# Performance work log

Hardware: AMD Instinct MI355X
Metric: run time of the kernel (lower is better)

Reference implementation:

```python
import jax, jax.numpy as jnp
import numpy as np

N_NODES = 50000
D = 128
L = 3  # layers
R = 4  # relations
E = 200000  # edges per relation
LN_EPS = 1e-5
NEG_SLOPE = 0.2


def setup_inputs() -> dict:
    key = jax.random.key(0)
    ks = jax.random.split(key, 12)
    s = 1.0 / np.sqrt(D)  # xavier-ish scale
    return {
        "h": jax.random.normal(ks[0], (N_NODES, D), jnp.float32),
        "edge_src": jax.random.randint(ks[1], (R, E), 0, N_NODES, jnp.int32),
        "edge_dst": jax.random.randint(ks[2], (R, E), 0, N_NODES, jnp.int32),
        "W_src": jax.random.normal(ks[3], (L, R, D, D), jnp.float32) * s,
        "W_dst": jax.random.normal(ks[4], (L, R, D, D), jnp.float32) * s,
        "attn_l": jax.random.normal(ks[5], (L, R, D), jnp.float32) * s,
        "attn_r": jax.random.normal(ks[6], (L, R, D), jnp.float32) * s,
        "gat_bias": jax.random.normal(ks[7], (L, R, D), jnp.float32) * 0.02,
        "ntype_bias": jax.random.normal(ks[8], (L, D), jnp.float32) * 0.02,
        "ln_gamma": jnp.ones((L, D), jnp.float32),
        "ln_beta": jnp.zeros((L, D), jnp.float32),
    }


def _gat_rel(x, Wsrc, Wdst, al, ar, b, src, dst):
    # single-head DGL GATConv with bipartite (src, dst) feats (same node set here)
    n = x.shape[0]
    hs = x @ Wsrc  # [N, D] projected source feats
    hd = x @ Wdst  # [N, D] projected dest feats
    el = (hs * al).sum(-1)  # [N]
    er = (hd * ar).sum(-1)  # [N]
    e = jax.nn.leaky_relu(el[src] + er[dst], NEG_SLOPE)  # [E]
    # edge softmax over incoming edges of each dst node
    m = jax.lax.stop_gradient(jax.ops.segment_max(e, dst, num_segments=n))
    a = jnp.exp(e - m[dst])
    denom = jax.ops.segment_sum(a, dst, num_segments=n)
    w = a / denom[dst]  # [E] attention weights
    out = jax.ops.segment_sum(hs[src] * w[:, None], dst, num_segments=n)  # [N, D]
    return out + b


def _layer_norm(x, g, b):
    mu = x.mean(-1, keepdims=True)
    var = ((x - mu) ** 2).mean(-1, keepdims=True)
    return (x - mu) * jax.lax.rsqrt(var + LN_EPS) * g + b


def reference(h, edge_src, edge_dst, W_src, W_dst, attn_l, attn_r,
              gat_bias, ntype_bias, ln_gamma, ln_beta):
    x = h
    n_layers = W_src.shape[0]
    gat_vmapped = jax.vmap(_gat_rel, in_axes=(None, 0, 0, 0, 0, 0, 0, 0))
    for l in range(n_layers):
        rel_out = gat_vmapped(x, W_src[l], W_dst[l], attn_l[l], attn_r[l],
                              gat_bias[l], edge_src, edge_dst)  # [R, N, D]
        hsum = rel_out.sum(0) + ntype_bias[l]  # HeteroGraphConv 'sum' + ntype bias
        if l < n_layers - 1:
            hsum = jax.nn.relu(hsum)  # activation on all but final layer
        # mean over heads (num_heads=1) is identity; then per-layer LayerNorm
        x = _layer_norm(hsum, ln_gamma[l], ln_beta[l])
    return x
```

## Files before the change

### kernel.cpp

```cpp
#include <hip/hip_runtime.h>

#define NN 50000
#define DIM 128
#define NREL 4
#define NEDGE 200000
#define NLAYER 3
#define SNB 196
#define NODES_PER_BLK 32

typedef short s16x8 __attribute__((ext_vector_type(8)));
typedef float f32x4 __attribute__((ext_vector_type(4)));

__device__ __forceinline__ unsigned short f2bf(float f) {
    union { float f; unsigned u; } c; c.f = f;
    unsigned u = c.u + 0x7fffu + ((c.u >> 16) & 1u);
    return (unsigned short)(u >> 16);
}
__device__ __forceinline__ float lo_bf(unsigned u) {
    union { float f; unsigned u; } c; c.u = u << 16; return c.f;
}
__device__ __forceinline__ float hi_bf(unsigned u) {
    union { float f; unsigned u; } c; c.u = u & 0xffff0000u; return c.f;
}

__global__ __launch_bounds__(256) void k_constf(float* __restrict__ out, int n, float v) {
    int i = blockIdx.x * 256 + threadIdx.x;
    if (i < n) out[i] = v;
}

__global__ __launch_bounds__(256) void k_count(const int* __restrict__ dst, int* __restrict__ counts) {
    int r = blockIdx.y;
    int i = blockIdx.x * 256 + threadIdx.x;
    if (i < NEDGE) {
        int d = dst[r * NEDGE + i];
        if ((unsigned)d < NN) atomicAdd(&counts[r * NN + d], 1);
    }
}

__global__ __launch_bounds__(256) void k_s1(const int* __restrict__ counts, int* __restrict__ bsum) {
    int r = blockIdx.y, b = blockIdx.x;
    int i = b * 256 + threadIdx.x;
    int v = (i < NN) ? counts[r * NN + i] : 0;
    #pragma unroll
    for (int m = 1; m < 64; m <<= 1) v += __shfl_xor(v, m);
    __shared__ int ws[4];
    int wid = threadIdx.x >> 6, lane = threadIdx.x & 63;
    if (lane == 0) ws[wid] = v;
    __syncthreads();
    if (threadIdx.x == 0) bsum[r * SNB + b] = ws[0] + ws[1] + ws[2] + ws[3];
}

__global__ __launch_bounds__(256) void k_s2(const int* __restrict__ bsum, int* __restrict__ boff) {
    int r = threadIdx.x >> 6;
    int lane = threadIdx.x & 63;
    int carry = 0;
    for (int c0 = 0; c0 < SNB; c0 += 64) {
        int b = c0 + lane;
        int v = (b < SNB) ? bsum[r * SNB + b] : 0;
        int inc = v;
        #pragma unroll
        for (int d = 1; d < 64; d <<= 1) {
            int t = __shfl_up(inc, d);
            if (lane >= d) inc += t;
        }
        if (b < SNB) boff[r * SNB + b] = carry + inc - v;
        carry += __shfl(inc, 63);
    }
}

__global__ __launch_bounds__(256) void k_s3(const int* __restrict__ counts, const int* __restrict__ boff,
                                            int* __restrict__ row_ptr, int* __restrict__ nxt) {
    int r = blockIdx.y, b = blockIdx.x;
    int i = b * 256 + threadIdx.x;
    int v = (i < NN) ? counts[r * NN + i] : 0;
    int lane = threadIdx.x & 63, wid = threadIdx.x >> 6;
    int inc = v;
    #pragma unroll
    for (int d = 1; d < 64; d <<= 1) {
        int t = __shfl_up(inc, d);
        if (lane >= d) inc += t;
    }
    __shared__ int ws[4];
    if (lane == 63) ws[wid] = inc;
    __syncthreads();
    int woff = 0;
    #pragma unroll
    for (int w = 0; w < 4; ++w) woff += (w < wid) ? ws[w] : 0;
    if (i < NN) {
        int ex = boff[r * SNB + b] + woff + inc - v;
        row_ptr[r * (NN + 1) + i] = ex;
        nxt[r * NN + i] = ex;
    }
    if (b == 0 && threadIdx.x == 0) row_ptr[r * (NN + 1) + NN] = NEDGE;
}

__global__ __launch_bounds__(256) void k_fill(const int* __restrict__ src, const int* __restrict__ dst,
                                              int* __restrict__ nxt, int* __restrict__ csr) {
    int r = blockIdx.y;
    int i = blockIdx.x * 256 + threadIdx.x;
    if (i < NEDGE) {
        int d = dst[r * NEDGE + i];
        if ((unsigned)d >= NN) return;
        int pos = atomicAdd(&nxt[r * NN + d], 1);
        if ((unsigned)pos < NEDGE) csr[r * NEDGE + pos] = src[r * NEDGE + i];
    }
}

__global__ __launch_bounds__(256) void k_prep(const float* __restrict__ Wsrc,
                                              const float* __restrict__ Wdst,
                                              const float* __restrict__ al,
                                              const float* __restrict__ ar,
                                              const float* __restrict__ ntb,
                                              const float* __restrict__ gb,
                                              const float* __restrict__ x,
                                              unsigned short* __restrict__ wf,
                                              float* __restrict__ wl,
                                              float* __restrict__ wr,
                                              float* __restrict__ biasc,
                                              unsigned short* __restrict__ xb) {
    int b = blockIdx.x;
    const int PL = NLAYER * 512;
    if (b < PL) {
        int l = b / 512;
        int t = b % 512;
        if (t < 256) {
            int idx = t * 256 + threadIdx.x;
            int jj = idx & 7, lane = (idx >> 3) & 63, s = (idx >> 9) & 3, tt = (idx >> 11) & 7, r = idx >> 14;
            int k = s * 32 + ((lane >> 4) << 3) + jj;
            int n = tt * 16 + (lane & 15);
            wf[l * 65536 + idx] = f2bf(Wsrc[((size_t)(l * NREL + r) * DIM + k) * DIM + n]);
        } else if (t < 384) {
            int gw = (t - 256) * 4 + (threadIdx.x >> 6);
            int lane = threadIdx.x & 63;
            int r = gw >> 7, k = gw & 127;
            const float* wrow = Wsrc + (((size_t)(l * NREL + r) * DIM + k) * DIM);
            const float* arow = al + (l * NREL + r) * DIM;
            float s = wrow[lane * 2] * arow[lane * 2] + wrow[lane * 2 + 1] * arow[lane * 2 + 1];
            #pragma unroll
            for (int m = 1; m < 64; m <<= 1) s += __shfl_xor(s, m);
            if (lane == 0) wl[l * 512 + gw] = s;
        } else {
            int gw = (t - 384) * 4 + (threadIdx.x >> 6);
            int lane = threadIdx.x & 63;
            int r = gw >> 7, k = gw & 127;
            const float* wrow = Wdst + (((size_t)(l * NREL + r) * DIM + k) * DIM);
            const float* arow = ar + (l * NREL + r) * DIM;
            float s = wrow[lane * 2] * arow[lane * 2] + wrow[lane * 2 + 1] * arow[lane * 2 + 1];
            #pragma unroll
            for (int m = 1; m < 64; m <<= 1) s += __shfl_xor(s, m);
            if (lane == 0) wr[l * 512 + gw] = s;
        }
    } else if (b < PL + 2) {
        int t = (b - PL) * 256 + threadIdx.x;
        if (t < NLAYER * DIM) {
            int l = t >> 7, k = t & 127;
            float s = ntb[t];
            #pragma unroll
            for (int r = 0; r < NREL; ++r) s += gb[(l * NREL + r) * DIM + k];
            biasc[t] = s;
        }
    } else {
        int i = ((b - PL - 2) * 256 + threadIdx.x) * 4;
        f32x4 v = *(const f32x4*)(x + i);
        unsigned short o[4];
        #pragma unroll
        for (int j = 0; j < 4; ++j) o[j] = f2bf(v[j]);
        *(ushort2*)(xb + i) = make_ushort2(o[0], o[1]);
        *(ushort2*)(xb + i + 2) = make_ushort2(o[2], o[3]);
    }
}

__global__ __launch_bounds__(256) void k_er0(const float* __restrict__ x,
                                             const float* __restrict__ wl,
                                             const float* __restrict__ wr,
                                             float* __restrict__ el,
                                             float* __restrict__ er) {
    int oct = threadIdx.x >> 3, ol = threadIdx.x & 7;
    int n = blockIdx.x * 32 + oct;
    if (n >= NN) return;
    int f0 = ol * 16;
    const float* xp = x + (size_t)n * DIM + f0;
    f32x4 xv[4];
    #pragma unroll
    for (int k = 0; k < 4; ++k) xv[k] = *(const f32x4*)(xp + 4 * k);
    #pragma unroll
    for (int r = 0; r < NREL; ++r) {
        float sl = 0.f, sr = 0.f;
        #pragma unroll
        for (int k = 0; k < 4; ++k) {
            f32x4 lv = *(const f32x4*)(wl + r * DIM + f0 + 4 * k);
            f32x4 rv = *(const f32x4*)(wr + r * DIM + f0 + 4 * k);
            sl += xv[k][0] * lv[0] + xv[k][1] * lv[1] + xv[k][2] * lv[2] + xv[k][3] * lv[3];
            sr += xv[k][0] * rv[0] + xv[k][1] * rv[1] + xv[k][2] * rv[2] + xv[k][3] * rv[3];
        }
        sl += __shfl_xor(sl, 1); sl += __shfl_xor(sl, 2); sl += __shfl_xor(sl, 4);
        sr += __shfl_xor(sr, 1); sr += __shfl_xor(sr, 2); sr += __shfl_xor(sr, 4);
        if (ol == 0) { el[r * NN + n] = sl; er[r * NN + n] = sr; }
    }
}

__global__ __launch_bounds__(256) void k_fused(const unsigned short* __restrict__ xb,
                                               const float* __restrict__ el,
                                               const float* __restrict__ er,
                                               const int* __restrict__ row_ptr,
                                               const int* __restrict__ csr,
                                               const unsigned short* __restrict__ wf,
                                               const float* __restrict__ biasc,
                                               const float* __restrict__ lng,
                                               const float* __restrict__ lnb,
                                               const float* __restrict__ wl,
                                               const float* __restrict__ wr,
                                               float* __restrict__ dout,
                                               unsigned short* __restrict__ xb2,
                                               float* __restrict__ el2,
                                               float* __restrict__ er2,
                                               int l, int last) {
    __shared__ s16x8 lds_a[2 * 16 * 64];
    int tid = threadIdx.x;

    for (int p = 0; p < 2; ++p) {
        int pair = tid >> 2;
        int ol   = tid & 3;
        int nd   = pair >> 2;
        int r    = pair & 3;
        int n    = blockIdx.x * NODES_PER_BLK + p * 16 + nd;
        int f0   = ol * 32;

        int valid = (n < NN);
        int nc = valid ? n : 0;
        int start = row_ptr[r * (NN + 1) + nc];
        int end   = valid ? row_ptr[r * (NN + 1) + nc + 1] : start;
        if (start < 0) start = 0;
        if (end > NEDGE) end = NEDGE;
        int deg = end - start;

        float ern = er[r * NN + nc];
        const int* cp = csr + r * NEDGE;
        const float* elp = el + r * NN;

        f32x4 av[8] = {{0,0,0,0},{0,0,0,0},{0,0,0,0},{0,0,0,0},
                       {0,0,0,0},{0,0,0,0},{0,0,0,0},{0,0,0,0}};
        float denom = 0.f;
        if (deg > 0) {
            int s0 = cp[start]; if ((unsigned)s0 >= NN) s0 = 0;
            float e0 = elp[s0];
            const uint4* hp = (const uint4*)(xb + (size_t)s0 * DIM + f0);
            uint4 xa = hp[0], xbv = hp[1], xc = hp[2], xd = hp[3];
            for (int e = 0; e < deg; ++e) {
                int i1 = start + e + 1; i1 = (i1 < end) ? i1 : start;
                int s1 = cp[i1]; if ((unsigned)s1 >= NN) s1 = 0;
                float e1 = elp[s1];
                const uint4* hp1 = (const uint4*)(xb + (size_t)s1 * DIM + f0);
                uint4 ya = hp1[0], yb = hp1[1], yc = hp1[2], yd = hp1[3];

                float ev = e0 + ern;
                ev = ev >= 0.f ? ev : 0.2f * ev;
                ev = fminf(fmaxf(ev, -60.f), 60.f);
                float pw = __expf(ev);
                denom += pw;
                av[0][0] += pw * lo_bf(xa.x); av[0][1] += pw * hi_bf(xa.x);
                av[0][2] += pw * lo_bf(xa.y); av[0][3] += pw * hi_bf(xa.y);
                av[1][0] += pw * lo_bf(xa.z); av[1][1] += pw * hi_bf(xa.z);
                av[1][2] += pw * lo_bf(xa.w); av[1][3] += pw * hi_bf(xa.w);
                av[2][0] += pw * lo_bf(xbv.x); av[2][1] += pw * hi_bf(xbv.x);
                av[2][2] += pw * lo_bf(xbv.y); av[2][3] += pw * hi_bf(xbv.y);
                av[3][0] += pw * lo_bf(xbv.z); av[3][1] += pw * hi_bf(xbv.z);
                av[3][2] += pw * lo_bf(xbv.w); av[3][3] += pw * hi_bf(xbv.w);
                av[4][0] += pw * lo_bf(xc.x); av[4][1] += pw * hi_bf(xc.x);
                av[4][2] += pw * lo_bf(xc.y); av[4][3] += pw * hi_bf(xc.y);
                av[5][0] += pw * lo_bf(xc.z); av[5][1] += pw * hi_bf(xc.z);
                av[5][2] += pw * lo_bf(xc.w); av[5][3] += pw * hi_bf(xc.w);
                av[6][0] += pw * lo_bf(xd.x); av[6][1] += pw * hi_bf(xd.x);
                av[6][2] += pw * lo_bf(xd.y); av[6][3] += pw * hi_bf(xd.y);
                av[7][0] += pw * lo_bf(xd.z); av[7][1] += pw * hi_bf(xd.z);
                av[7][2] += pw * lo_bf(xd.w); av[7][3] += pw * hi_bf(xd.w);
                e0 = e1; xa = ya; xbv = yb; xc = yc; xd = yd;
            }
        }
        float inv = (deg > 0) ? (1.0f / denom) : 0.f;
        #pragma unroll
        for (int q = 0; q < 4; ++q) {
            s16x8 o;
            #pragma unroll
            for (int j = 0; j < 4; ++j) {
                o[j]     = (short)f2bf(av[2 * q][j] * inv);
                o[j + 4] = (short)f2bf(av[2 * q + 1][j] * inv);
            }
            lds_a[p * 1024 + (r * 4 + ol) * 64 + q * 16 + nd] = o;
        }
    }
    __syncthreads();

    int wv = tid >> 6, lane = tid & 63;
    int quad = lane >> 4, n16 = lane & 15;
    f32x4 acc00 = {0.f, 0.f, 0.f, 0.f}, acc01 = {0.f, 0.f, 0.f, 0.f};
    f32x4 acc10 = {0.f, 0.f, 0.f, 0.f}, acc11 = {0.f, 0.f, 0.f, 0.f};
    {
        const s16x8* wfp = (const s16x8*)wf + (size_t)l * NREL * 2048;
        int t0c = wv * 2, t1c = wv * 2 + 1;
        #pragma unroll
        for (int sp = 0; sp < 16; ++sp) {
            s16x8 a0 = lds_a[sp * 64 + lane];
            s16x8 a1 = lds_a[1024 + sp * 64 + lane];
            const s16x8* wb = wfp + (size_t)(sp >> 2) * 2048;
            int sl = sp & 3;
            s16x8 b0 = wb[(t0c * 4 + sl) * 64 + lane];
            s16x8 b1 = wb[(t1c * 4 + sl) * 64 + lane];
            acc00 = __builtin_amdgcn_mfma_f32_16x16x32_bf16(a0, b0, acc00, 0, 0, 0);
            acc01 = __builtin_amdgcn_mfma_f32_16x16x32_bf16(a0, b1, acc01, 0, 0, 0);
            acc10 = __builtin_amdgcn_mfma_f32_16x16x32_bf16(a1, b0, acc10, 0, 0, 0);
            acc11 = __builtin_amdgcn_mfma_f32_16x16x32_bf16(a1, b1, acc11, 0, 0, 0);
        }
    }
    __syncthreads();
    float* Cl = (float*)lds_a;
    {
        int t0c = wv * 2, t1c = wv * 2 + 1;
        #pragma unroll
        for (int reg = 0; reg < 4; ++reg) {
            int row = quad * 4 + reg;
            Cl[row * DIM + t0c * 16 + n16] = acc00[reg];
            Cl[row * DIM + t1c * 16 + n16] = acc01[reg];
            Cl[(16 + row) * DIM + t0c * 16 + n16] = acc10[reg];
            Cl[(16 + row) * DIM + t1c * 16 + n16] = acc11[reg];
        }
    }
    __syncthreads();

    for (int it = 0; it < 4; ++it) {
        int nd2 = it * 8 + (tid >> 5);
        int sub = tid & 31;
        int f   = sub * 4;
        int n2  = blockIdx.x * NODES_PER_BLK + nd2;
        if (n2 >= NN) continue;

        float t[4];
        #pragma unroll
        for (int j = 0; j < 4; ++j) t[j] = Cl[nd2 * DIM + f + j] + biasc[l * DIM + f + j];
        if (!last) {
            #pragma unroll
            for (int j = 0; j < 4; ++j) t[j] = fmaxf(t[j], 0.f);
        }
        float s1 = 0.f;
        #pragma unroll
        for (int j = 0; j < 4; ++j) s1 += t[j];
        s1 += __shfl_xor(s1, 1); s1 += __shfl_xor(s1, 2);
        s1 += __shfl_xor(s1, 4); s1 += __shfl_xor(s1, 8);
        s1 += __shfl_xor(s1, 16);
        float mean = s1 * (1.0f / 128.0f);
        float s2 = 0.f;
        #pragma unroll
        for (int j = 0; j < 4; ++j) { t[j] -= mean; s2 += t[j] * t[j]; }
        s2 += __shfl_xor(s2, 1); s2 += __shfl_xor(s2, 2);
        s2 += __shfl_xor(s2, 4); s2 += __shfl_xor(s2, 8);
        s2 += __shfl_xor(s2, 16);
        float rs = rsqrtf(s2 * (1.0f / 128.0f) + 1e-5f);

        float y[4];
        #pragma unroll
        for (int j = 0; j < 4; ++j)
            y[j] = t[j] * rs * lng[l * DIM + f + j] + lnb[l * DIM + f + j];

        if (last) {
            float* op = dout + (size_t)n2 * DIM + f;
            f32x4 v0;
            v0[0] = y[0]; v0[1] = y[1]; v0[2] = y[2]; v0[3] = y[3];
            *(f32x4*)op = v0;
        } else {
            unsigned pk0 = (unsigned)f2bf(y[0]) | ((unsigned)f2bf(y[1]) << 16);
            unsigned pk1 = (unsigned)f2bf(y[2]) | ((unsigned)f2bf(y[3]) << 16);
            uint2 v; v.x = pk0; v.y = pk1;
            *(uint2*)(xb2 + (size_t)n2 * DIM + f) = v;

            const float* wlp = wl + (l + 1) * 512;
            const float* wrp = wr + (l + 1) * 512;
            #pragma unroll
            for (int rp = 0; rp < NREL; ++rp) {
                float sl_ = 0.f, sr_ = 0.f;
                #pragma unroll
                for (int j = 0; j < 4; ++j) {
                    sl_ += y[j] * wlp[rp * DIM + f + j];
                    sr_ += y[j] * wrp[rp * DIM + f + j];
                }
                sl_ += __shfl_xor(sl_, 1); sl_ += __shfl_xor(sl_, 2);
                sl_ += __shfl_xor(sl_, 4); sl_ += __shfl_xor(sl_, 8);
                sl_ += __shfl_xor(sl_, 16);
                sr_ += __shfl_xor(sr_, 1); sr_ += __shfl_xor(sr_, 2);
                sr_ += __shfl_xor(sr_, 4); sr_ += __shfl_xor(sr_, 8);
                sr_ += __shfl_xor(sr_, 16);
                if (sub == 0) {
                    el2[rp * NN + n2] = sl_;
                    er2[rp * NN + n2] = sr_;
                }
            }
        }
    }
}

extern "C" void kernel_launch(void* const* d_in, const int* in_sizes, int n_in,
                              void* d_out, int out_size, void* d_ws, size_t ws_size,
                              hipStream_t stream) {
    const float* h        = (const float*)d_in[0];
    const int*   edge_src = (const int*)d_in[1];
    const int*   edge_dst = (const int*)d_in[2];
    const float* W_src    = (const float*)d_in[3];
    const float* W_dst    = (const float*)d_in[4];
    const float* attn_l   = (const float*)d_in[5];
    const float* attn_r   = (const float*)d_in[6];
    const float* gat_bias = (const float*)d_in[7];
    const float* ntype_b  = (const float*)d_in[8];
    const float* ln_g     = (const float*)d_in[9];
    const float* ln_b     = (const float*)d_in[10];

    if (n_in < 11) return;
    if (in_sizes[0] != NN * DIM) return;
    if (in_sizes[1] != NREL * NEDGE || in_sizes[2] != NREL * NEDGE) return;
    if (in_sizes[3] != NLAYER * NREL * DIM * DIM || in_sizes[4] != NLAYER * NREL * DIM * DIM) return;
    if (in_sizes[5] != NLAYER * NREL * DIM || in_sizes[6] != NLAYER * NREL * DIM) return;
    if (in_sizes[7] != NLAYER * NREL * DIM || in_sizes[8] != NLAYER * DIM) return;
    if (out_size != NN * DIM) return;

    auto align256 = [](size_t x) { return (x + 255) & ~(size_t)255; };
    size_t szElEr = align256((size_t)NREL * NN * 4);
    size_t szXbf  = align256((size_t)NN * DIM * 2);
    size_t szWlr  = align256((size_t)NLAYER * 512 * 4);
    size_t szBc   = align256((size_t)NLAYER * DIM * 4);
    size_t szWf   = align256((size_t)NLAYER * NREL * DIM * DIM * 2);
    size_t szRp   = align256((size_t)NREL * (NN + 1) * 4);
    size_t szNxt  = align256((size_t)NREL * NN * 4);
    size_t szCsr  = align256((size_t)NREL * NEDGE * 4);
    size_t szScn  = align256((size_t)NREL * SNB * 4) * 2;
    size_t need = 4 * szElEr + 2 * szXbf + 2 * szWlr + szBc + szWf + szRp + szNxt + szCsr + szScn;

    if (ws_size < need) {
        k_constf<<<(NN * DIM + 255) / 256, 256, 0, stream>>>((float*)d_out, NN * DIM, 100.0f);
        return;
    }

    char* base = (char*)d_ws;
    size_t off = 0;
    auto alloc = [&](size_t bytes) -> char* { char* p = base + off; off += align256(bytes); return p; };

    float* el   = (float*)alloc((size_t)NREL * NN * 4);
    float* er   = (float*)alloc((size_t)NREL * NN * 4);
    float* el2  = (float*)alloc((size_t)NREL * NN * 4);
    float* er2  = (float*)alloc((size_t)NREL * NN * 4);
    unsigned short* xbf  = (unsigned short*)alloc((size_t)NN * DIM * 2);
    unsigned short* xbf2 = (unsigned short*)alloc((size_t)NN * DIM * 2);
    float* wl    = (float*)alloc((size_t)NLAYER * 512 * 4);
    float* wr    = (float*)alloc((size_t)NLAYER * 512 * 4);
    float* biasc = (float*)alloc((size_t)NLAYER * DIM * 4);
    unsigned short* wfrag = (unsigned short*)alloc((size_t)NLAYER * NREL * DIM * DIM * 2);
    int* rowp = (int*)alloc((size_t)NREL * (NN + 1) * 4);
    int* nxt  = (int*)alloc((size_t)NREL * NN * 4);
    int* csr  = (int*)alloc((size_t)NREL * NEDGE * 4);
    int* bsum = (int*)alloc((size_t)NREL * SNB * 4);
    int* boff = (int*)alloc((size_t)NREL * SNB * 4);

    (void)hipMemsetAsync(nxt, 0, (size_t)NREL * NN * 4, stream);
    k_count<<<dim3((NEDGE + 255) / 256, NREL), 256, 0, stream>>>(edge_dst, nxt);
    k_s1<<<dim3(SNB, NREL), 256, 0, stream>>>(nxt, bsum);
    k_s2<<<1, 256, 0, stream>>>(bsum, boff);
    k_s3<<<dim3(SNB, NREL), 256, 0, stream>>>(nxt, boff, rowp, nxt);
    k_fill<<<dim3((NEDGE + 255) / 256, NREL), 256, 0, stream>>>(edge_src, edge_dst, nxt, csr);
    k_prep<<<NLAYER * 512 + 2 + NN * DIM / 1024, 256, 0, stream>>>(
        W_src, W_dst, attn_l, attn_r, ntype_b, gat_bias, h, wfrag, wl, wr, biasc, xbf);
    k_er0<<<(NN + 31) / 32, 256, 0, stream>>>(h, wl, wr, el, er);

    float* dout = (float*)d_out;
    int nblk = (NN + NODES_PER_BLK - 1) / NODES_PER_BLK;
    k_fused<<<nblk, 256, 0, stream>>>(xbf, el, er, rowp, csr, wfrag, biasc, ln_g, ln_b,
                                      wl, wr, dout, xbf2, el2, er2, 0, 0);
    k_fused<<<nblk, 256, 0, stream>>>(xbf2, el2, er2, rowp, csr, wfrag, biasc, ln_g, ln_b,
                                      wl, wr, dout, xbf, el, er, 1, 0);
    k_fused<<<nblk, 256, 0, stream>>>(xbf, el, er, rowp, csr, wfrag, biasc, ln_g, ln_b,
                                      wl, wr, dout, xbf2, el2, er2, 2, 1);
}
```

Measured before the change: 367.6 us.

## Split fused gather+GEMM kernel into separate gather and large-tile GEMM kernels

```diff
diff --git a/kernel.cpp b/kernel.cpp
--- a/kernel.cpp
+++ b/kernel.cpp
@@ -6,7 +6,8 @@
 #define NEDGE 200000
 #define NLAYER 3
 #define SNB 196
-#define NODES_PER_BLK 32
+#define GR 128
+#define NTILE (NN / 16)
 
 typedef short s16x8 __attribute__((ext_vector_type(8)));
 typedef float f32x4 __attribute__((ext_vector_type(4)));
@@ -199,139 +200,145 @@
     }
 }
 
-__global__ __launch_bounds__(256) void k_fused(const unsigned short* __restrict__ xb,
-                                               const float* __restrict__ el,
-                                               const float* __restrict__ er,
-                                               const int* __restrict__ row_ptr,
-                                               const int* __restrict__ csr,
-                                               const unsigned short* __restrict__ wf,
-                                               const float* __restrict__ biasc,
-                                               const float* __restrict__ lng,
-                                               const float* __restrict__ lnb,
-                                               const float* __restrict__ wl,
-                                               const float* __restrict__ wr,
-                                               float* __restrict__ dout,
-                                               unsigned short* __restrict__ xb2,
-                                               float* __restrict__ el2,
-                                               float* __restrict__ er2,
-                                               int l, int last) {
-    __shared__ s16x8 lds_a[2 * 16 * 64];
+__global__ __launch_bounds__(256) void k_gather(const unsigned short* __restrict__ xb,
+                                                const float* __restrict__ el,
+                                                const float* __restrict__ er,
+                                                const int* __restrict__ row_ptr,
+                                                const int* __restrict__ csr,
+                                                unsigned short* __restrict__ aggf) {
+    int gid = blockIdx.x * 256 + threadIdx.x;
+    int ol = gid & 3;
+    int p  = gid >> 2;
+    int n  = p >> 2;
+    int r  = p & 3;
+    if (n >= NN) return;
+    int f0 = ol * 32;
+
+    int start = row_ptr[r * (NN + 1) + n];
+    int end   = row_ptr[r * (NN + 1) + n + 1];
+    if (start < 0) start = 0;
+    if (end > NEDGE) end = NEDGE;
+    int deg = end - start;
+
+    float ern = er[r * NN + n];
+    const int* cp = csr + r * NEDGE;
+    const float* elp = el + r * NN;
+
+    f32x4 av[8] = {{0,0,0,0},{0,0,0,0},{0,0,0,0},{0,0,0,0},
+                   {0,0,0,0},{0,0,0,0},{0,0,0,0},{0,0,0,0}};
+    float denom = 0.f;
+    if (deg > 0) {
+        int s0 = cp[start]; if ((unsigned)s0 >= NN) s0 = 0;
+        float e0 = elp[s0];
+        const uint4* hp = (const uint4*)(xb + (size_t)s0 * DIM + f0);
+        uint4 xa = hp[0], xbv = hp[1], xc = hp[2], xd = hp[3];
+        for (int e = 0; e < deg; ++e) {
+            int i1 = start + e + 1; i1 = (i1 < end) ? i1 : start;
+            int s1 = cp[i1]; if ((unsigned)s1 >= NN) s1 = 0;
+            float e1 = elp[s1];
+            const uint4* hp1 = (const uint4*)(xb + (size_t)s1 * DIM + f0);
+            uint4 ya = hp1[0], yb = hp1[1], yc = hp1[2], yd = hp1[3];
+
+            float ev = e0 + ern;
+            ev = ev >= 0.f ? ev : 0.2f * ev;
+            ev = fminf(fmaxf(ev, -60.f), 60.f);
+            float pw = __expf(ev);
+            denom += pw;
+            av[0][0] += pw * lo_bf(xa.x); av[0][1] += pw * hi_bf(xa.x);
+            av[0][2] += pw * lo_bf(xa.y); av[0][3] += pw * hi_bf(xa.y);
+            av[1][0] += pw * lo_bf(xa.z); av[1][1] += pw * hi_bf(xa.z);
+            av[1][2] += pw * lo_bf(xa.w); av[1][3] += pw * hi_bf(xa.w);
+            av[2][0] += pw * lo_bf(xbv.x); av[2][1] += pw * hi_bf(xbv.x);
+            av[2][2] += pw * lo_bf(xbv.y); av[2][3] += pw * hi_bf(xbv.y);
+            av[3][0] += pw * lo_bf(xbv.z); av[3][1] += pw * hi_bf(xbv.z);
+            av[3][2] += pw * lo_bf(xbv.w); av[3][3] += pw * hi_bf(xbv.w);
+            av[4][0] += pw * lo_bf(xc.x); av[4][1] += pw * hi_bf(xc.x);
+            av[4][2] += pw * lo_bf(xc.y); av[4][3] += pw * hi_bf(xc.y);
+            av[5][0] += pw * lo_bf(xc.z); av[5][1] += pw * hi_bf(xc.z);
+            av[5][2] += pw * lo_bf(xc.w); av[5][3] += pw * hi_bf(xc.w);
+            av[6][0] += pw * lo_bf(xd.x); av[6][1] += pw * hi_bf(xd.x);
+            av[6][2] += pw * lo_bf(xd.y); av[6][3] += pw * hi_bf(xd.y);
+            av[7][0] += pw * lo_bf(xd.z); av[7][1] += pw * hi_bf(xd.z);
+            av[7][2] += pw * lo_bf(xd.w); av[7][3] += pw * hi_bf(xd.w);
+            e0 = e1; xa = ya; xbv = yb; xc = yc; xd = yd;
+        }
+    }
+    float inv = (deg > 0) ? (1.0f / denom) : 0.f;
+    s16x8* ap = (s16x8*)aggf + ((size_t)(n >> 4) * 16 + (r * 4 + ol)) * 64 + (n & 15);
+    #pragma unroll
+    for (int q = 0; q < 4; ++q) {
+        s16x8 o;
+        #pragma unroll
+        for (int j = 0; j < 4; ++j) {
+            o[j]     = (short)f2bf(av[2 * q][j] * inv);
+            o[j + 4] = (short)f2bf(av[2 * q + 1][j] * inv);
+        }
+        ap[q * 16] = o;
+    }
+}
+
+__global__ __launch_bounds__(256) void k_gemm(const unsigned short* __restrict__ aggf,
+                                              const unsigned short* __restrict__ wf,
+                                              const float* __restrict__ biasc,
+                                              const float* __restrict__ lng,
+                                              const float* __restrict__ lnb,
+                                              const float* __restrict__ wl,
+                                              const float* __restrict__ wr,
+                                              float* __restrict__ dout,
+                                              unsigned short* __restrict__ xb2,
+                                              float* __restrict__ el2,
+                                              float* __restrict__ er2,
+                                              int l, int last) {
+    __shared__ float Cl[GR * DIM];
     int tid = threadIdx.x;
-
-    for (int p = 0; p < 2; ++p) {
-        int pair = tid >> 2;
-        int ol   = tid & 3;
-        int nd   = pair >> 2;
-        int r    = pair & 3;
-        int n    = blockIdx.x * NODES_PER_BLK + p * 16 + nd;
-        int f0   = ol * 32;
-
-        int valid = (n < NN);
-        int nc = valid ? n : 0;
-        int start = row_ptr[r * (NN + 1) + nc];
-        int end   = valid ? row_ptr[r * (NN + 1) + nc + 1] : start;
-        if (start < 0) start = 0;
-        if (end > NEDGE) end = NEDGE;
-        int deg = end - start;
-
-        float ern = er[r * NN + nc];
-        const int* cp = csr + r * NEDGE;
-        const float* elp = el + r * NN;
-
-        f32x4 av[8] = {{0,0,0,0},{0,0,0,0},{0,0,0,0},{0,0,0,0},
-                       {0,0,0,0},{0,0,0,0},{0,0,0,0},{0,0,0,0}};
-        float denom = 0.f;
-        if (deg > 0) {
-            int s0 = cp[start]; if ((unsigned)s0 >= NN) s0 = 0;
-            float e0 = elp[s0];
-            const uint4* hp = (const uint4*)(xb + (size_t)s0 * DIM + f0);
-            uint4 xa = hp[0], xbv = hp[1], xc = hp[2], xd = hp[3];
-            for (int e = 0; e < deg; ++e) {
-                int i1 = start + e + 1; i1 = (i1 < end) ? i1 : start;
-                int s1 = cp[i1]; if ((unsigned)s1 >= NN) s1 = 0;
-                float e1 = elp[s1];
-                const uint4* hp1 = (const uint4*)(xb + (size_t)s1 * DIM + f0);
-                uint4 ya = hp1[0], yb = hp1[1], yc = hp1[2], yd = hp1[3];
-
-                float ev = e0 + ern;
-                ev = ev >= 0.f ? ev : 0.2f * ev;
-                ev = fminf(fmaxf(ev, -60.f), 60.f);
-                float pw = __expf(ev);
-                denom += pw;
-                av[0][0] += pw * lo_bf(xa.x); av[0][1] += pw * hi_bf(xa.x);
-                av[0][2] += pw * lo_bf(xa.y); av[0][3] += pw * hi_bf(xa.y);
-                av[1][0] += pw * lo_bf(xa.z); av[1][1] += pw * hi_bf(xa.z);
-                av[1][2] += pw * lo_bf(xa.w); av[1][3] += pw * hi_bf(xa.w);
-                av[2][0] += pw * lo_bf(xbv.x); av[2][1] += pw * hi_bf(xbv.x);
-                av[2][2] += pw * lo_bf(xbv.y); av[2][3] += pw * hi_bf(xbv.y);
-                av[3][0] += pw * lo_bf(xbv.z); av[3][1] += pw * hi_bf(xbv.z);
-                av[3][2] += pw * lo_bf(xbv.w); av[3][3] += pw * hi_bf(xbv.w);
-                av[4][0] += pw * lo_bf(xc.x); av[4][1] += pw * hi_bf(xc.x);
-                av[4][2] += pw * lo_bf(xc.y); av[4][3] += pw * hi_bf(xc.y);
-                av[5][0] += pw * lo_bf(xc.z); av[5][1] += pw * hi_bf(xc.z);
-                av[5][2] += pw * lo_bf(xc.w); av[5][3] += pw * hi_bf(xc.w);
-                av[6][0] += pw * lo_bf(xd.x); av[6][1] += pw * hi_bf(xd.x);
-                av[6][2] += pw * lo_bf(xd.y); av[6][3] += pw * hi_bf(xd.y);
-                av[7][0] += pw * lo_bf(xd.z); av[7][1] += pw * hi_bf(xd.z);
-                av[7][2] += pw * lo_bf(xd.w); av[7][3] += pw * hi_bf(xd.w);
-                e0 = e1; xa = ya; xbv = yb; xc = yc; xd = yd;
-            }
-        }
-        float inv = (deg > 0) ? (1.0f / denom) : 0.f;
-        #pragma unroll
-        for (int q = 0; q < 4; ++q) {
-            s16x8 o;
-            #pragma unroll
-            for (int j = 0; j < 4; ++j) {
-                o[j]     = (short)f2bf(av[2 * q][j] * inv);
-                o[j + 4] = (short)f2bf(av[2 * q + 1][j] * inv);
-            }
-            lds_a[p * 1024 + (r * 4 + ol) * 64 + q * 16 + nd] = o;
-        }
-    }
-    __syncthreads();
-
     int wv = tid >> 6, lane = tid & 63;
     int quad = lane >> 4, n16 = lane & 15;
-    f32x4 acc00 = {0.f, 0.f, 0.f, 0.f}, acc01 = {0.f, 0.f, 0.f, 0.f};
-    f32x4 acc10 = {0.f, 0.f, 0.f, 0.f}, acc11 = {0.f, 0.f, 0.f, 0.f};
+    int tile0 = blockIdx.x * (GR / 16);
+
+    f32x4 acc0[8], acc1[8];
+    #pragma unroll
+    for (int rt = 0; rt < 8; ++rt) {
+        acc0[rt] = (f32x4){0.f, 0.f, 0.f, 0.f};
+        acc1[rt] = (f32x4){0.f, 0.f, 0.f, 0.f};
+    }
     {
         const s16x8* wfp = (const s16x8*)wf + (size_t)l * NREL * 2048;
+        const s16x8* af = (const s16x8*)aggf;
         int t0c = wv * 2, t1c = wv * 2 + 1;
-        #pragma unroll
         for (int sp = 0; sp < 16; ++sp) {
-            s16x8 a0 = lds_a[sp * 64 + lane];
-            s16x8 a1 = lds_a[1024 + sp * 64 + lane];
             const s16x8* wb = wfp + (size_t)(sp >> 2) * 2048;
             int sl = sp & 3;
             s16x8 b0 = wb[(t0c * 4 + sl) * 64 + lane];
             s16x8 b1 = wb[(t1c * 4 + sl) * 64 + lane];
-            acc00 = __builtin_amdgcn_mfma_f32_16x16x32_bf16(a0, b0, acc00, 0, 0, 0);
-            acc01 = __builtin_amdgcn_mfma_f32_16x16x32_bf16(a0, b1, acc01, 0, 0, 0);
-            acc10 = __builtin_amdgcn_mfma_f32_16x16x32_bf16(a1, b0, acc10, 0, 0, 0);
-            acc11 = __builtin_amdgcn_mfma_f32_16x16x32_bf16(a1, b1, acc11, 0, 0, 0);
-        }
-    }
-    __syncthreads();
-    float* Cl = (float*)lds_a;
+            #pragma unroll
+            for (int rt = 0; rt < 8; ++rt) {
+                int tile = tile0 + rt;
+                if (tile >= NTILE) tile = 0;
+                s16x8 a = af[((size_t)tile * 16 + sp) * 64 + lane];
+                acc0[rt] = __builtin_amdgcn_mfma_f32_16x16x32_bf16(a, b0, acc0[rt], 0, 0, 0);
+                acc1[rt] = __builtin_amdgcn_mfma_f32_16x16x32_bf16(a, b1, acc1[rt], 0, 0, 0);
+            }
+        }
+    }
     {
         int t0c = wv * 2, t1c = wv * 2 + 1;
         #pragma unroll
-        for (int reg = 0; reg < 4; ++reg) {
-            int row = quad * 4 + reg;
-            Cl[row * DIM + t0c * 16 + n16] = acc00[reg];
-            Cl[row * DIM + t1c * 16 + n16] = acc01[reg];
-            Cl[(16 + row) * DIM + t0c * 16 + n16] = acc10[reg];
-            Cl[(16 + row) * DIM + t1c * 16 + n16] = acc11[reg];
+        for (int rt = 0; rt < 8; ++rt) {
+            #pragma unroll
+            for (int reg = 0; reg < 4; ++reg) {
+                int row = rt * 16 + quad * 4 + reg;
+                Cl[row * DIM + t0c * 16 + n16] = acc0[rt][reg];
+                Cl[row * DIM + t1c * 16 + n16] = acc1[rt][reg];
+            }
         }
     }
     __syncthreads();
 
-    for (int it = 0; it < 4; ++it) {
+    for (int it = 0; it < GR / 8; ++it) {
         int nd2 = it * 8 + (tid >> 5);
         int sub = tid & 31;
         int f   = sub * 4;
-        int n2  = blockIdx.x * NODES_PER_BLK + nd2;
+        int n2  = blockIdx.x * GR + nd2;
         if (n2 >= NN) continue;
 
         float t[4];
@@ -430,7 +437,8 @@
     size_t szNxt  = align256((size_t)NREL * NN * 4);
     size_t szCsr  = align256((size_t)NREL * NEDGE * 4);
     size_t szScn  = align256((size_t)NREL * SNB * 4) * 2;
-    size_t need = 4 * szElEr + 2 * szXbf + 2 * szWlr + szBc + szWf + szRp + szNxt + szCsr + szScn;
+    size_t szAgg  = align256((size_t)NN * 512 * 2);
+    size_t need = 4 * szElEr + 2 * szXbf + 2 * szWlr + szBc + szWf + szRp + szNxt + szCsr + szScn + szAgg;
 
     if (ws_size < need) {
         k_constf<<<(NN * DIM + 255) / 256, 256, 0, stream>>>((float*)d_out, NN * DIM, 100.0f);
@@ -456,6 +464,7 @@
     int* csr  = (int*)alloc((size_t)NREL * NEDGE * 4);
     int* bsum = (int*)alloc((size_t)NREL * SNB * 4);
     int* boff = (int*)alloc((size_t)NREL * SNB * 4);
+    unsigned short* aggf = (unsigned short*)alloc((size_t)NN * 512 * 2);
 
     (void)hipMemsetAsync(nxt, 0, (size_t)NREL * NN * 4, stream);
     k_count<<<dim3((NEDGE + 255) / 256, NREL), 256, 0, stream>>>(edge_dst, nxt);
@@ -468,11 +477,16 @@
     k_er0<<<(NN + 31) / 32, 256, 0, stream>>>(h, wl, wr, el, er);
 
     float* dout = (float*)d_out;
-    int nblk = (NN + NODES_PER_BLK - 1) / NODES_PER_BLK;
-    k_fused<<<nblk, 256, 0, stream>>>(xbf, el, er, rowp, csr, wfrag, biasc, ln_g, ln_b,
-                                      wl, wr, dout, xbf2, el2, er2, 0, 0);
-    k_fused<<<nblk, 256, 0, stream>>>(xbf2, el2, er2, rowp, csr, wfrag, biasc, ln_g, ln_b,
-                                      wl, wr, dout, xbf, el, er, 1, 0);
-    k_fused<<<nblk, 256, 0, stream>>>(xbf, el, er, rowp, csr, wfrag, biasc, ln_g, ln_b,
-                                      wl, wr, dout, xbf2, el2, er2, 2, 1);
-}
+    const int GATHER_BLK = (NN * NREL * 4 + 255) / 256;
+    const int GEMM_BLK   = (NN + GR - 1) / GR;
+
+    k_gather<<<GATHER_BLK, 256, 0, stream>>>(xbf, el, er, rowp, csr, aggf);
+    k_gemm<<<GEMM_BLK, 256, 0, stream>>>(aggf, wfrag, biasc, ln_g, ln_b, wl, wr,
+                                         dout, xbf2, el2, er2, 0, 0);
+    k_gather<<<GATHER_BLK, 256, 0, stream>>>(xbf2, el2, er2, rowp, csr, aggf);
+    k_gemm<<<GEMM_BLK, 256, 0, stream>>>(aggf, wfrag, biasc, ln_g, ln_b, wl, wr,
+                                         dout, xbf, el, er, 1, 0);
+    k_gather<<<GATHER_BLK, 256, 0, stream>>>(xbf, el, er, rowp, csr, aggf);
+    k_gemm<<<GEMM_BLK, 256, 0, stream>>>(aggf, wfrag, biasc, ln_g, ln_b, wl, wr,
+                                         dout, xbf2, el2, er2, 2, 1);
+}
```

After: 434.2 us. +18.1%, slower.
